# Kernel tuning notes

Measured on AMD Instinct MI355X. Metric: run time of the kernel, lower is better.

## Reference

```python
import jax, jax.numpy as jnp
import numpy as np

EPS = 1e-5  # equinox LayerNorm default eps

def setup_inputs() -> dict:
    key = jax.random.key(0)
    k1, k2, k3, k4, k5 = jax.random.split(key, 5)
    heads, d, dH, N = 16, 1024, 64, 2048
    # lecun-normal-ish scaling for fan_in=d
    s = 1.0 / np.sqrt(d)
    return {
        "x": jax.random.normal(k1, (d, N), dtype=jnp.float32),
        "WQ": jax.random.normal(k2, (heads, d, dH), dtype=jnp.float32) * s,
        "WK": jax.random.normal(k3, (heads, d, dH), dtype=jnp.float32) * s,
        "WV": jax.random.normal(k4, (heads, d, dH), dtype=jnp.float32) * s,
        "W0": jax.random.normal(k5, (d, d), dtype=jnp.float32) * s,
    }

def reference(x, WQ, WK, WV, W0):
    # x: [d, N]
    residual = x
    # equinox LayerNorm over full shape (d, N), no affine params
    mean = jnp.mean(x)
    var = jnp.var(x)
    xn = (x - mean) * jax.lax.rsqrt(var + EPS)
    # project: [h, d_model, dH] x [d_model, N] -> [h, dH, N]
    Q = jnp.einsum('hcd,ci->hdi', WQ, xn)
    K = jnp.einsum('hcd,ci->hdi', WK, xn)
    V = jnp.einsum('hcd,ci->hdi', WV, xn)
    dH = WK.shape[-1]
    dot = jnp.einsum('hdi,hdj->hij', Q, K)  # [h, N, N]
    alpha = jax.nn.softmax(dot / jnp.sqrt(jnp.asarray(dH, dot.dtype)), axis=-1)
    attn = jnp.einsum('hij,hdj->hdi', alpha, V)  # [h, dH, N]
    N = attn.shape[2]
    attn = attn.reshape(-1, N)  # [d, N]
    out = W0 @ attn
    return out + residual
```

## Files before the change

### kernel.cpp

```cpp
#include <hip/hip_runtime.h>
#include <math.h>

typedef unsigned short u16;
typedef _Float16 f16;
typedef __attribute__((ext_vector_type(8))) short bf16x8;
typedef __attribute__((ext_vector_type(4))) float f32x4;
typedef __attribute__((ext_vector_type(4))) f16 f16x4;

#define D_MODEL 1024
#define SEQ_N   2048
#define HEADS   16
#define DHEAD   64
#define M3      3072
#define NIT     (SEQ_N / 64)

#define GLOBAL_AS __attribute__((address_space(1)))
#define LDS_AS    __attribute__((address_space(3)))
#define ASYNC16(gp, lp) __builtin_amdgcn_global_load_lds( \
    (const GLOBAL_AS unsigned int*)(gp), (LDS_AS unsigned int*)(lp), 16, 0, 0)

__device__ __forceinline__ u16 f2bf(float f) {
  union { float f; unsigned int u; } v; v.f = f;
  unsigned int r = v.u + 0x7fffu + ((v.u >> 16) & 1u);
  return (u16)(r >> 16);
}

__global__ __launch_bounds__(256) void prep(const float* __restrict__ x,
                                            double* __restrict__ part,
                                            const float* __restrict__ WQ,
                                            const float* __restrict__ WK,
                                            const float* __restrict__ WV,
                                            const float* __restrict__ W0,
                                            u16* __restrict__ Wp,
                                            u16* __restrict__ W0p) {
  __shared__ double ls[256], lss[256];
  __shared__ float tile[32][65];
  int t = threadIdx.x;
  int b = blockIdx.x;
  if (b < 256) {
    const float4* x4 = (const float4*)x;
    const int n4 = (D_MODEL * SEQ_N) / 4;
    double s = 0.0, ss = 0.0;
    for (int idx = b * 256 + t; idx < n4; idx += 256 * 256) {
      float4 v = x4[idx];
      s  += (double)v.x + (double)v.y + (double)v.z + (double)v.w;
      ss += (double)v.x * v.x + (double)v.y * v.y + (double)v.z * v.z + (double)v.w * v.w;
    }
    ls[t] = s; lss[t] = ss;
    __syncthreads();
    for (int off = 128; off > 0; off >>= 1) {
      if (t < off) { ls[t] += ls[t + off]; lss[t] += lss[t + off]; }
      __syncthreads();
    }
    if (t == 0) { part[2 * b] = ls[0]; part[2 * b + 1] = lss[0]; }
    return;
  }
  int f = b - 256;
  int z = f >> 9;
  int rem = f & 511;
  if (z == 3) {
    int idx = rem * 512 + t;
#pragma unroll
    for (int r = 0; r < 2; ++r, idx += 256) {
      float4 v = ((const float4*)W0)[idx];
      unsigned int lo = (unsigned int)f2bf(v.x) | ((unsigned int)f2bf(v.y) << 16);
      unsigned int hi = (unsigned int)f2bf(v.z) | ((unsigned int)f2bf(v.w) << 16);
      uint2 o; o.x = lo; o.y = hi;
      *(uint2*)(&W0p[(size_t)idx * 4]) = o;
    }
    return;
  }
  const float* W = (z == 0) ? WQ : ((z == 1) ? WK : WV);
  int h = rem >> 5, cb = (rem & 31) * 32;
  int dh = t & 63, cl = t >> 6;
  for (int r = 0; r < 8; ++r) {
    int c = cl + r * 4;
    tile[c][dh] = W[((size_t)h * D_MODEL + cb + c) * DHEAD + dh];
  }
  __syncthreads();
  int c2 = t & 31, d2 = t >> 5;
  for (int r = 0; r < 8; ++r) {
    int dd = d2 + r * 8;
    Wp[(size_t)((z * HEADS + h) * DHEAD + dd) * D_MODEL + cb + c2] = f2bf(tile[c2][dd]);
  }
}

__global__ __launch_bounds__(256) void ln_norm_t(const float* __restrict__ x,
                                                 const double* __restrict__ part,
                                                 u16* __restrict__ xnt) {
  __shared__ double ls[256], lss[256];
  __shared__ float tile[64][65];
  int t = threadIdx.x;
  ls[t] = part[2 * t]; lss[t] = part[2 * t + 1];
  __syncthreads();
  for (int off = 128; off > 0; off >>= 1) {
    if (t < off) { ls[t] += ls[t + off]; lss[t] += lss[t + off]; }
    __syncthreads();
  }
  double inv = 1.0 / ((double)D_MODEL * (double)SEQ_N);
  double m = ls[0] * inv;
  double vv = lss[0] * inv - m * m;
  float mean = (float)m;
  float rstd = (float)(1.0 / sqrt(vv + 1e-5));

  int ib = blockIdx.x * 64, cb = blockIdx.y * 64;
  int il = t & 63, cl = t >> 6;
  for (int r = 0; r < 16; ++r) {
    int c = cl + r * 4;
    tile[c][il] = (x[(size_t)(cb + c) * SEQ_N + ib + il] - mean) * rstd;
  }
  __syncthreads();
  int c2 = t & 63, i2 = t >> 6;
  for (int r = 0; r < 16; ++r) {
    int i = i2 + r * 4;
    xnt[(size_t)(ib + i) * D_MODEL + cb + c2] = f2bf(tile[c2][i]);
  }
}

__global__ __launch_bounds__(256) void gemm_qkv(const u16* __restrict__ A,
                                                const u16* __restrict__ Bt,
                                                u16* __restrict__ Qt,
                                                u16* __restrict__ Kt,
                                                f16* __restrict__ Vb) {
  __shared__ __align__(16) u16 Alds[2 * 2 * 96 * 32];
  __shared__ __align__(16) u16 Blds[2 * 2 * 128 * 32];
  int t = threadIdx.x;
  int lane = t & 63, w = t >> 6;
  int g = lane >> 4, l16 = lane & 15;
  int wr = w >> 1, wc = w & 1;
  int flat = blockIdx.x;
  int wi = flat >> 3;
  int wx = wi & 7, wy = wi >> 3;
  int cx = (flat & 7) & 1, cy = (flat & 7) >> 1;
  int bx = cx * 8 + wx;
  int by = cy * 8 + wy;
  int mb = by * 96, nb = bx * 128;

  f32x4 acc[3][4];
#pragma unroll
  for (int i = 0; i < 3; ++i)
#pragma unroll
    for (int j = 0; j < 4; ++j) acc[i][j] = (f32x4){0.f, 0.f, 0.f, 0.f};

  const u16* AgP[3]; int ldsA[3];
#pragma unroll
  for (int r = 0; r < 3; ++r) {
    int idx = r * 256 + t;
    int kk = (idx >= 384) ? 1 : 0;
    int rem = idx - kk * 384;
    int row = rem >> 2, c4 = rem & 3;
    AgP[r] = A + (size_t)(mb + row) * D_MODEL + kk * 32 + c4 * 8;
    ldsA[r] = idx * 8;
  }
  const u16* BgP[4]; int ldsB[4];
#pragma unroll
  for (int r = 0; r < 4; ++r) {
    int idx = r * 256 + t;
    int kk = idx >> 9;
    int rem = idx & 511;
    int row = rem >> 2, c4 = rem & 3;
    BgP[r] = Bt + (size_t)(nb + row) * D_MODEL + kk * 32 + c4 * 8;
    ldsB[r] = idx * 8;
  }

#pragma unroll
  for (int r = 0; r < 3; ++r) ASYNC16(AgP[r], &Alds[ldsA[r]]);
#pragma unroll
  for (int r = 0; r < 4; ++r) ASYNC16(BgP[r], &Blds[ldsB[r]]);
#pragma unroll
  for (int r = 0; r < 3; ++r) ASYNC16(AgP[r] + 64, &Alds[6144 + ldsA[r]]);
#pragma unroll
  for (int r = 0; r < 4; ++r) ASYNC16(BgP[r] + 64, &Blds[8192 + ldsB[r]]);

  int cur = 0;
  for (int ks = 0; ks < 16; ++ks) {
    if (ks < 15) asm volatile("s_waitcnt vmcnt(7)" ::: "memory");
    else         asm volatile("s_waitcnt vmcnt(0)" ::: "memory");
    __builtin_amdgcn_s_barrier();
#pragma unroll
    for (int kk = 0; kk < 2; ++kk) {
      bf16x8 af[3], bf[4];
#pragma unroll
      for (int tm = 0; tm < 3; ++tm)
        af[tm] = *(const bf16x8*)(&Alds[cur * 6144 + kk * 3072 +
                                        (wr * 48 + tm * 16 + l16) * 32 + g * 8]);
#pragma unroll
      for (int tn = 0; tn < 4; ++tn)
        bf[tn] = *(const bf16x8*)(&Blds[cur * 8192 + kk * 4096 +
                                        (wc * 64 + tn * 16 + l16) * 32 + g * 8]);
#pragma unroll
      for (int tm = 0; tm < 3; ++tm)
#pragma unroll
        for (int tn = 0; tn < 4; ++tn)
          acc[tm][tn] = __builtin_amdgcn_mfma_f32_16x16x32_bf16(af[tm], bf[tn],
                                                                acc[tm][tn], 0, 0, 0);
    }
    __builtin_amdgcn_s_barrier();
    if (ks + 2 < 16) {
      int kb = (ks + 2) * 64;
#pragma unroll
      for (int r = 0; r < 3; ++r) ASYNC16(AgP[r] + kb, &Alds[cur * 6144 + ldsA[r]]);
#pragma unroll
      for (int r = 0; r < 4; ++r) ASYNC16(BgP[r] + kb, &Blds[cur * 8192 + ldsB[r]]);
    }
    cur ^= 1;
  }

#pragma unroll
  for (int tm = 0; tm < 3; ++tm) {
    int row0 = mb + wr * 48 + tm * 16 + g * 4;
#pragma unroll
    for (int tn = 0; tn < 4; ++tn) {
      int col = nb + wc * 64 + tn * 16 + l16;
      if (row0 < 2 * D_MODEL) {
        u16* T = (row0 < D_MODEL) ? Qt : Kt;
        int rbase = (row0 < D_MODEL) ? row0 : row0 - D_MODEL;
        ushort4 o;
        o.x = f2bf(acc[tm][tn][0]); o.y = f2bf(acc[tm][tn][1]);
        o.z = f2bf(acc[tm][tn][2]); o.w = f2bf(acc[tm][tn][3]);
        *(ushort4*)(&T[(size_t)col * D_MODEL + rbase]) = o;
      } else {
        int rbase = row0 - 2 * D_MODEL;
#pragma unroll
        for (int r = 0; r < 4; ++r)
          Vb[(size_t)(rbase + r) * SEQ_N + col] = (f16)acc[tm][tn][r];
      }
    }
  }
}

__global__ __launch_bounds__(256) void gemm_bf16(const u16* __restrict__ A,
                                                 const u16* __restrict__ Bt,
                                                 float* __restrict__ C,
                                                 const float* __restrict__ res,
                                                 int M, int N, int K) {
  __shared__ __align__(16) u16 Alds[2 * 2 * 64 * 32];
  __shared__ __align__(16) u16 Blds[2 * 2 * 64 * 32];
  int t = threadIdx.x;
  int w = t >> 6, lane = t & 63;
  int g = lane >> 4, l16 = lane & 15;
  int flat = blockIdx.x;
  int wi = flat >> 3;
  int wx = wi & 7, wy = wi >> 3;
  int cx = (flat & 7) & 3, cy = (flat & 7) >> 2;
  int bx = cx * 8 + wx;
  int by = cy * 8 + wy;
  int mb = by * 64, nb = bx * 64;
  f32x4 acc[4];
  for (int i = 0; i < 4; ++i) acc[i] = (f32x4){0.f, 0.f, 0.f, 0.f};

  const u16* AgP[2]; const u16* BgP[2]; int ldsO[2];
#pragma unroll
  for (int r = 0; r < 2; ++r) {
    int idx = r * 256 + t;
    int kk = idx >> 8;
    int rem = idx & 255;
    int row = rem >> 2, c4 = rem & 3;
    AgP[r] = A + (size_t)(mb + row) * K + kk * 32 + c4 * 8;
    BgP[r] = Bt + (size_t)(nb + row) * K + kk * 32 + c4 * 8;
    ldsO[r] = idx * 8;
  }

#pragma unroll
  for (int r = 0; r < 2; ++r) { ASYNC16(AgP[r], &Alds[ldsO[r]]); ASYNC16(BgP[r], &Blds[ldsO[r]]); }
#pragma unroll
  for (int r = 0; r < 2; ++r) {
    ASYNC16(AgP[r] + 64, &Alds[4096 + ldsO[r]]);
    ASYNC16(BgP[r] + 64, &Blds[4096 + ldsO[r]]);
  }

  int cur = 0;
  const int NK = 16;
  for (int ks = 0; ks < NK; ++ks) {
    if (ks < NK - 1) asm volatile("s_waitcnt vmcnt(4)" ::: "memory");
    else             asm volatile("s_waitcnt vmcnt(0)" ::: "memory");
    __builtin_amdgcn_s_barrier();
#pragma unroll
    for (int kk = 0; kk < 2; ++kk) {
      bf16x8 af = *(const bf16x8*)(&Alds[cur * 4096 + kk * 2048 + (w * 16 + l16) * 32 + g * 8]);
#pragma unroll
      for (int tn = 0; tn < 4; ++tn) {
        bf16x8 bf = *(const bf16x8*)(&Blds[cur * 4096 + kk * 2048 + (tn * 16 + l16) * 32 + g * 8]);
        acc[tn] = __builtin_amdgcn_mfma_f32_16x16x32_bf16(af, bf, acc[tn], 0, 0, 0);
      }
    }
    __builtin_amdgcn_s_barrier();
    if (ks + 2 < NK) {
      int kb = (ks + 2) * 64;
#pragma unroll
      for (int r = 0; r < 2; ++r) {
        ASYNC16(AgP[r] + kb, &Alds[cur * 4096 + ldsO[r]]);
        ASYNC16(BgP[r] + kb, &Blds[cur * 4096 + ldsO[r]]);
      }
    }
    cur ^= 1;
  }
  int col0 = nb + l16;
  int row0 = mb + w * 16 + g * 4;
#pragma unroll
  for (int tn = 0; tn < 4; ++tn) {
    int col = col0 + tn * 16;
#pragma unroll
    for (int r = 0; r < 4; ++r) {
      int row = row0 + r;
      float v = acc[tn][r];
      if (res) v += res[(size_t)row * N + col];
      C[(size_t)row * N + col] = v;
    }
  }
}

__global__ __launch_bounds__(256, 2) void attn_mfma(const u16* __restrict__ Qt,
                                                    const u16* __restrict__ Kt,
                                                    const f16* __restrict__ Vb,
                                                    u16* __restrict__ attnt) {
  __shared__ __align__(16) u16 Klds[2][64][72];
  __shared__ __align__(16) f16 Vlds[2][64][72];
  int flat = blockIdx.x;
  int xcd = flat & 7, idx = flat >> 3;
  int h  = xcd * 2 + (idx >> 5);
  int ib = (idx & 31) * 64;
  int t = threadIdx.x;
  int w = t >> 6, lane = t & 63;
  int g = lane >> 4, l16 = lane & 15;

  bf16x8 bq[2];
  {
    const u16* qb = Qt + (size_t)(ib + w * 16 + l16) * D_MODEL + h * DHEAD + g * 8;
    bq[0] = *(const bf16x8*)(qb);
    bq[1] = *(const bf16x8*)(qb + 32);
  }

  f32x4 acc_o[4];
#pragma unroll
  for (int i = 0; i < 4; ++i) acc_o[i] = (f32x4){0.f, 0.f, 0.f, 0.f};
  f32x4 acc_l = (f32x4){0.f, 0.f, 0.f, 0.f};
  f16x4 ones;
  ones[0] = (f16)1.f; ones[1] = (f16)1.f; ones[2] = (f16)1.f; ones[3] = (f16)1.f;

  int srow = t >> 2, sc0 = (t & 3) * 16;
  const u16* Kg = Kt + (size_t)srow * D_MODEL + h * DHEAD + sc0;
  const f16* Vg = Vb + (size_t)(h * DHEAD + srow) * SEQ_N + sc0;

  uint4 ka = *(const uint4*)(Kg);
  uint4 kb = *(const uint4*)(Kg + 8);
  uint4 va = *(const uint4*)(Vg);
  uint4 vb = *(const uint4*)(Vg + 8);
  *(uint4*)(&Klds[0][srow][sc0]) = ka;
  *(uint4*)(&Klds[0][srow][sc0 + 8]) = kb;
  *(uint4*)(&Vlds[0][srow][sc0]) = va;
  *(uint4*)(&Vlds[0][srow][sc0 + 8]) = vb;
  __syncthreads();

  int cur = 0;
  for (int it = 0; it < NIT; ++it) {
    if (it + 1 < NIT) {
      const u16* Kn = Kg + (size_t)(it + 1) * 64 * D_MODEL;
      const f16* Vn = Vg + (it + 1) * 64;
      ka = *(const uint4*)(Kn);
      kb = *(const uint4*)(Kn + 8);
      va = *(const uint4*)(Vn);
      vb = *(const uint4*)(Vn + 8);
    }

    f32x4 s[4];
#pragma unroll
    for (int i = 0; i < 4; ++i) s[i] = (f32x4){0.f, 0.f, 0.f, 0.f};
    __builtin_amdgcn_s_setprio(1);
#pragma unroll
    for (int kk = 0; kk < 2; ++kk)
#pragma unroll
      for (int tn = 0; tn < 4; ++tn) {
        bf16x8 ak = *(const bf16x8*)(&Klds[cur][tn * 16 + l16][kk * 32 + g * 8]);
        s[tn] = __builtin_amdgcn_mfma_f32_16x16x32_bf16(ak, bq[kk], s[tn], 0, 0, 0);
      }
    __builtin_amdgcn_s_setprio(0);
    f16x4 pf[4];
#pragma unroll
    for (int tn = 0; tn < 4; ++tn) {
      f16x4 p;
#pragma unroll
      for (int r = 0; r < 4; ++r)
        p[r] = (f16)__expf(fmaf(s[tn][r], 0.125f, -4.0f));
      pf[tn] = p;
    }
    __builtin_amdgcn_s_setprio(1);
#pragma unroll
    for (int tn = 0; tn < 4; ++tn) {
      acc_l = __builtin_amdgcn_mfma_f32_16x16x16f16(pf[tn], ones, acc_l, 0, 0, 0);
#pragma unroll
      for (int td = 0; td < 4; ++td) {
        f16x4 bv = *(const f16x4*)(&Vlds[cur][td * 16 + l16][tn * 16 + g * 4]);
        acc_o[td] =
            __builtin_amdgcn_mfma_f32_16x16x16f16(pf[tn], bv, acc_o[td], 0, 0, 0);
      }
    }
    __builtin_amdgcn_s_setprio(0);

    if (it + 1 < NIT) {
      *(uint4*)(&Klds[cur ^ 1][srow][sc0]) = ka;
      *(uint4*)(&Klds[cur ^ 1][srow][sc0 + 8]) = kb;
      *(uint4*)(&Vlds[cur ^ 1][srow][sc0]) = va;
      *(uint4*)(&Vlds[cur ^ 1][srow][sc0 + 8]) = vb;
    }
    __syncthreads();
    cur ^= 1;
  }

  float inv0 = 1.0f / acc_l[0];
  float inv1 = 1.0f / acc_l[1];
  float inv2 = 1.0f / acc_l[2];
  float inv3 = 1.0f / acc_l[3];
#pragma unroll
  for (int td = 0; td < 4; ++td) {
    int dh = h * DHEAD + td * 16 + l16;
    int i0 = ib + w * 16 + g * 4;
    attnt[(size_t)(i0 + 0) * D_MODEL + dh] = f2bf(acc_o[td][0] * inv0);
    attnt[(size_t)(i0 + 1) * D_MODEL + dh] = f2bf(acc_o[td][1] * inv1);
    attnt[(size_t)(i0 + 2) * D_MODEL + dh] = f2bf(acc_o[td][2] * inv2);
    attnt[(size_t)(i0 + 3) * D_MODEL + dh] = f2bf(acc_o[td][3] * inv3);
  }
}

extern "C" void kernel_launch(void* const* d_in, const int* in_sizes, int n_in,
                              void* d_out, int out_size, void* d_ws, size_t ws_size,
                              hipStream_t stream) {
  const float* x  = (const float*)d_in[0];
  const float* WQ = (const float*)d_in[1];
  const float* WK = (const float*)d_in[2];
  const float* WV = (const float*)d_in[3];
  const float* W0 = (const float*)d_in[4];
  float* out = (float*)d_out;

  char* ws = (char*)d_ws;
  size_t off = 0;
  double* part  = (double*)(ws + off); off += 8192;
  u16*    xnt   = (u16*)(ws + off); off += (size_t)SEQ_N * D_MODEL * 2;
  u16*    Wp    = (u16*)(ws + off); off += (size_t)M3 * D_MODEL * 2;
  u16*    W0p   = (u16*)(ws + off); off += (size_t)D_MODEL * D_MODEL * 2;
  u16*    Qt    = (u16*)(ws + off); off += (size_t)SEQ_N * D_MODEL * 2;
  u16*    Kt    = (u16*)(ws + off); off += (size_t)SEQ_N * D_MODEL * 2;
  f16*    Vb    = (f16*)(ws + off); off += (size_t)D_MODEL * SEQ_N * 2;
  u16*    attnt = (u16*)(ws + off); off += (size_t)SEQ_N * D_MODEL * 2;

  prep<<<256 + 2048, 256, 0, stream>>>(x, part, WQ, WK, WV, W0, Wp, W0p);
  ln_norm_t<<<dim3(SEQ_N / 64, D_MODEL / 64), 256, 0, stream>>>(x, part, xnt);
  gemm_qkv<<<512, 256, 0, stream>>>(Wp, xnt, Qt, Kt, Vb);
  attn_mfma<<<512, 256, 0, stream>>>(Qt, Kt, Vb, attnt);
  gemm_bf16<<<512, 256, 0, stream>>>(W0p, attnt, out, x, D_MODEL, SEQ_N, D_MODEL);
}
```

Before: 152.9 us.

## Fuse all five stages into one cooperative persistent kernel with grid syncs

Replaces the five separate kernel launches (stats/weight prep, layernorm transpose, QKV GEMM, attention, output GEMM) with a single cooperative kernel of 512 blocks that separates the stages with grid.sync(). The prep stage is reshaped so 512 blocks cover the stats and weight conversion work formerly spread over 2304 blocks. The aim is to remove per-launch overhead and the gaps between dependent kernels. In exchange, each stage is limited to 512 resident blocks with launch bounds allowing 2 per CU and a shared 56KB LDS buffer, and grid-wide barriers add their own cost. The old multi-kernel path is kept as a fallback if the cooperative launch fails.

```diff
diff --git a/kernel.cpp b/kernel.cpp
--- a/kernel.cpp
+++ b/kernel.cpp
@@ -1,5 +1,8 @@
 #include <hip/hip_runtime.h>
+#include <hip/hip_cooperative_groups.h>
 #include <math.h>
+
+namespace cg = cooperative_groups;
 
 typedef unsigned short u16;
 typedef _Float16 f16;
@@ -23,6 +26,406 @@
   union { float f; unsigned int u; } v; v.f = f;
   unsigned int r = v.u + 0x7fffu + ((v.u >> 16) & 1u);
   return (u16)(r >> 16);
+}
+
+__global__ __launch_bounds__(256, 2) void fused(
+    const float* __restrict__ x,  const float* __restrict__ WQ,
+    const float* __restrict__ WK, const float* __restrict__ WV,
+    const float* __restrict__ W0, float* __restrict__ out,
+    double* __restrict__ part, u16* __restrict__ xnt,
+    u16* __restrict__ Wp, u16* __restrict__ W0p,
+    u16* __restrict__ Qt, u16* __restrict__ Kt,
+    f16* __restrict__ Vb, u16* __restrict__ attnt) {
+  __shared__ __align__(16) char smem[57344];
+  cg::grid_group grid = cg::this_grid();
+  int b = blockIdx.x;
+  int t = threadIdx.x;
+
+  {
+    double* ls  = (double*)smem;
+    double* lss = ls + 256;
+    float*  tile = (float*)(smem + 4096);
+    if (b < 256) {
+      const float4* x4 = (const float4*)x;
+      const int n4 = (D_MODEL * SEQ_N) / 4;
+      double s = 0.0, ss = 0.0;
+      for (int idx = b * 256 + t; idx < n4; idx += 256 * 256) {
+        float4 v = x4[idx];
+        s  += (double)v.x + (double)v.y + (double)v.z + (double)v.w;
+        ss += (double)v.x * v.x + (double)v.y * v.y + (double)v.z * v.z + (double)v.w * v.w;
+      }
+      ls[t] = s; lss[t] = ss;
+      __syncthreads();
+      for (int off = 128; off > 0; off >>= 1) {
+        if (t < off) { ls[t] += ls[t + off]; lss[t] += lss[t + off]; }
+        __syncthreads();
+      }
+      if (t == 0) { part[2 * b] = ls[0]; part[2 * b + 1] = lss[0]; }
+    } else {
+      int base = (b - 256) * 8;
+      int z = base >> 9;
+      if (z == 3) {
+#pragma unroll
+        for (int u = 0; u < 8; ++u) {
+          int rem = (base + u) & 511;
+          int idx = rem * 512 + t;
+#pragma unroll
+          for (int r = 0; r < 2; ++r, idx += 256) {
+            float4 v = ((const float4*)W0)[idx];
+            unsigned int lo = (unsigned int)f2bf(v.x) | ((unsigned int)f2bf(v.y) << 16);
+            unsigned int hi = (unsigned int)f2bf(v.z) | ((unsigned int)f2bf(v.w) << 16);
+            uint2 o; o.x = lo; o.y = hi;
+            *(uint2*)(&W0p[(size_t)idx * 4]) = o;
+          }
+        }
+      } else {
+        const float* W = (z == 0) ? WQ : ((z == 1) ? WK : WV);
+        for (int u = 0; u < 8; ++u) {
+          int rem = (base + u) & 511;
+          int h = rem >> 5, cb = (rem & 31) * 32;
+          int dh = t & 63, cl = t >> 6;
+          for (int r = 0; r < 8; ++r) {
+            int c = cl + r * 4;
+            tile[c * 65 + dh] = W[((size_t)h * D_MODEL + cb + c) * DHEAD + dh];
+          }
+          __syncthreads();
+          int c2 = t & 31, d2 = t >> 5;
+          for (int r = 0; r < 8; ++r) {
+            int dd = d2 + r * 8;
+            Wp[(size_t)((z * HEADS + h) * DHEAD + dd) * D_MODEL + cb + c2] =
+                f2bf(tile[c2 * 65 + dd]);
+          }
+          __syncthreads();
+        }
+      }
+    }
+  }
+  grid.sync();
+
+  {
+    double* ls  = (double*)smem;
+    double* lss = ls + 256;
+    float*  tile = (float*)(smem + 4096);
+    ls[t] = part[2 * t]; lss[t] = part[2 * t + 1];
+    __syncthreads();
+    for (int off = 128; off > 0; off >>= 1) {
+      if (t < off) { ls[t] += ls[t + off]; lss[t] += lss[t + off]; }
+      __syncthreads();
+    }
+    double inv = 1.0 / ((double)D_MODEL * (double)SEQ_N);
+    double m = ls[0] * inv;
+    double vv = lss[0] * inv - m * m;
+    float mean = (float)m;
+    float rstd = (float)(1.0 / sqrt(vv + 1e-5));
+
+    int ib = (b & 31) * 64, cb = (b >> 5) * 64;
+    int il = t & 63, cl = t >> 6;
+    for (int r = 0; r < 16; ++r) {
+      int c = cl + r * 4;
+      tile[c * 65 + il] = (x[(size_t)(cb + c) * SEQ_N + ib + il] - mean) * rstd;
+    }
+    __syncthreads();
+    int c2 = t & 63, i2 = t >> 6;
+    for (int r = 0; r < 16; ++r) {
+      int i = i2 + r * 4;
+      xnt[(size_t)(ib + i) * D_MODEL + cb + c2] = f2bf(tile[c2 * 65 + i]);
+    }
+  }
+  grid.sync();
+
+  {
+    u16* Alds = (u16*)smem;
+    u16* Blds = (u16*)(smem + 24576);
+    int lane = t & 63, w = t >> 6;
+    int g = lane >> 4, l16 = lane & 15;
+    int wr = w >> 1, wc = w & 1;
+    int wi = b >> 3;
+    int wx = wi & 7, wy = wi >> 3;
+    int cx = (b & 7) & 1, cy = (b & 7) >> 1;
+    int bx = cx * 8 + wx;
+    int by = cy * 8 + wy;
+    int mb = by * 96, nb = bx * 128;
+
+    f32x4 acc[3][4];
+#pragma unroll
+    for (int i = 0; i < 3; ++i)
+#pragma unroll
+      for (int j = 0; j < 4; ++j) acc[i][j] = (f32x4){0.f, 0.f, 0.f, 0.f};
+
+    const u16* AgP[3]; int ldsA[3];
+#pragma unroll
+    for (int r = 0; r < 3; ++r) {
+      int idx = r * 256 + t;
+      int kk = (idx >= 384) ? 1 : 0;
+      int rem = idx - kk * 384;
+      int row = rem >> 2, c4 = rem & 3;
+      AgP[r] = Wp + (size_t)(mb + row) * D_MODEL + kk * 32 + c4 * 8;
+      ldsA[r] = idx * 8;
+    }
+    const u16* BgP[4]; int ldsB[4];
+#pragma unroll
+    for (int r = 0; r < 4; ++r) {
+      int idx = r * 256 + t;
+      int kk = idx >> 9;
+      int rem = idx & 511;
+      int row = rem >> 2, c4 = rem & 3;
+      BgP[r] = xnt + (size_t)(nb + row) * D_MODEL + kk * 32 + c4 * 8;
+      ldsB[r] = idx * 8;
+    }
+
+#pragma unroll
+    for (int r = 0; r < 3; ++r) ASYNC16(AgP[r], &Alds[ldsA[r]]);
+#pragma unroll
+    for (int r = 0; r < 4; ++r) ASYNC16(BgP[r], &Blds[ldsB[r]]);
+#pragma unroll
+    for (int r = 0; r < 3; ++r) ASYNC16(AgP[r] + 64, &Alds[6144 + ldsA[r]]);
+#pragma unroll
+    for (int r = 0; r < 4; ++r) ASYNC16(BgP[r] + 64, &Blds[8192 + ldsB[r]]);
+
+    int cur = 0;
+    for (int ks = 0; ks < 16; ++ks) {
+      if (ks < 15) asm volatile("s_waitcnt vmcnt(7)" ::: "memory");
+      else         asm volatile("s_waitcnt vmcnt(0)" ::: "memory");
+      __builtin_amdgcn_s_barrier();
+#pragma unroll
+      for (int kk = 0; kk < 2; ++kk) {
+        bf16x8 af[3], bf[4];
+#pragma unroll
+        for (int tm = 0; tm < 3; ++tm)
+          af[tm] = *(const bf16x8*)(&Alds[cur * 6144 + kk * 3072 +
+                                          (wr * 48 + tm * 16 + l16) * 32 + g * 8]);
+#pragma unroll
+        for (int tn = 0; tn < 4; ++tn)
+          bf[tn] = *(const bf16x8*)(&Blds[cur * 8192 + kk * 4096 +
+                                          (wc * 64 + tn * 16 + l16) * 32 + g * 8]);
+#pragma unroll
+        for (int tm = 0; tm < 3; ++tm)
+#pragma unroll
+          for (int tn = 0; tn < 4; ++tn)
+            acc[tm][tn] = __builtin_amdgcn_mfma_f32_16x16x32_bf16(af[tm], bf[tn],
+                                                                  acc[tm][tn], 0, 0, 0);
+      }
+      __builtin_amdgcn_s_barrier();
+      if (ks + 2 < 16) {
+        int kb = (ks + 2) * 64;
+#pragma unroll
+        for (int r = 0; r < 3; ++r) ASYNC16(AgP[r] + kb, &Alds[cur * 6144 + ldsA[r]]);
+#pragma unroll
+        for (int r = 0; r < 4; ++r) ASYNC16(BgP[r] + kb, &Blds[cur * 8192 + ldsB[r]]);
+      }
+      cur ^= 1;
+    }
+
+#pragma unroll
+    for (int tm = 0; tm < 3; ++tm) {
+      int row0 = mb + wr * 48 + tm * 16 + g * 4;
+#pragma unroll
+      for (int tn = 0; tn < 4; ++tn) {
+        int col = nb + wc * 64 + tn * 16 + l16;
+        if (row0 < 2 * D_MODEL) {
+          u16* T = (row0 < D_MODEL) ? Qt : Kt;
+          int rbase = (row0 < D_MODEL) ? row0 : row0 - D_MODEL;
+          ushort4 o;
+          o.x = f2bf(acc[tm][tn][0]); o.y = f2bf(acc[tm][tn][1]);
+          o.z = f2bf(acc[tm][tn][2]); o.w = f2bf(acc[tm][tn][3]);
+          *(ushort4*)(&T[(size_t)col * D_MODEL + rbase]) = o;
+        } else {
+          int rbase = row0 - 2 * D_MODEL;
+#pragma unroll
+          for (int r = 0; r < 4; ++r)
+            Vb[(size_t)(rbase + r) * SEQ_N + col] = (f16)acc[tm][tn][r];
+        }
+      }
+    }
+  }
+  grid.sync();
+
+  {
+    u16* Klds = (u16*)smem;
+    f16* Vlds = (f16*)(smem + 18432);
+#define KLD(bf_, r_, c_) Klds[(bf_)*4608 + (r_)*72 + (c_)]
+#define VLD(bf_, r_, c_) Vlds[(bf_)*4608 + (r_)*72 + (c_)]
+    int xcd = b & 7, idx = b >> 3;
+    int h  = xcd * 2 + (idx >> 5);
+    int ib = (idx & 31) * 64;
+    int w = t >> 6, lane = t & 63;
+    int g = lane >> 4, l16 = lane & 15;
+
+    bf16x8 bq[2];
+    {
+      const u16* qb = Qt + (size_t)(ib + w * 16 + l16) * D_MODEL + h * DHEAD + g * 8;
+      bq[0] = *(const bf16x8*)(qb);
+      bq[1] = *(const bf16x8*)(qb + 32);
+    }
+
+    f32x4 acc_o[4];
+#pragma unroll
+    for (int i = 0; i < 4; ++i) acc_o[i] = (f32x4){0.f, 0.f, 0.f, 0.f};
+    f32x4 acc_l = (f32x4){0.f, 0.f, 0.f, 0.f};
+    f16x4 ones;
+    ones[0] = (f16)1.f; ones[1] = (f16)1.f; ones[2] = (f16)1.f; ones[3] = (f16)1.f;
+
+    int srow = t >> 2, sc0 = (t & 3) * 16;
+    const u16* Kg = Kt + (size_t)srow * D_MODEL + h * DHEAD + sc0;
+    const f16* Vg = Vb + (size_t)(h * DHEAD + srow) * SEQ_N + sc0;
+
+    uint4 ka = *(const uint4*)(Kg);
+    uint4 kb = *(const uint4*)(Kg + 8);
+    uint4 va = *(const uint4*)(Vg);
+    uint4 vb = *(const uint4*)(Vg + 8);
+    *(uint4*)(&KLD(0, srow, sc0)) = ka;
+    *(uint4*)(&KLD(0, srow, sc0 + 8)) = kb;
+    *(uint4*)(&VLD(0, srow, sc0)) = va;
+    *(uint4*)(&VLD(0, srow, sc0 + 8)) = vb;
+    __syncthreads();
+
+    int cur = 0;
+    for (int it = 0; it < NIT; ++it) {
+      if (it + 1 < NIT) {
+        const u16* Kn = Kg + (size_t)(it + 1) * 64 * D_MODEL;
+        const f16* Vn = Vg + (it + 1) * 64;
+        ka = *(const uint4*)(Kn);
+        kb = *(const uint4*)(Kn + 8);
+        va = *(const uint4*)(Vn);
+        vb = *(const uint4*)(Vn + 8);
+      }
+
+      f32x4 s[4];
+#pragma unroll
+      for (int i = 0; i < 4; ++i) s[i] = (f32x4){0.f, 0.f, 0.f, 0.f};
+      __builtin_amdgcn_s_setprio(1);
+#pragma unroll
+      for (int kk = 0; kk < 2; ++kk)
+#pragma unroll
+        for (int tn = 0; tn < 4; ++tn) {
+          bf16x8 ak = *(const bf16x8*)(&KLD(cur, tn * 16 + l16, kk * 32 + g * 8));
+          s[tn] = __builtin_amdgcn_mfma_f32_16x16x32_bf16(ak, bq[kk], s[tn], 0, 0, 0);
+        }
+      __builtin_amdgcn_s_setprio(0);
+      f16x4 pf[4];
+#pragma unroll
+      for (int tn = 0; tn < 4; ++tn) {
+        f16x4 p;
+#pragma unroll
+        for (int r = 0; r < 4; ++r)
+          p[r] = (f16)__expf(fmaf(s[tn][r], 0.125f, -4.0f));
+        pf[tn] = p;
+      }
+      __builtin_amdgcn_s_setprio(1);
+#pragma unroll
+      for (int tn = 0; tn < 4; ++tn) {
+        acc_l = __builtin_amdgcn_mfma_f32_16x16x16f16(pf[tn], ones, acc_l, 0, 0, 0);
+#pragma unroll
+        for (int td = 0; td < 4; ++td) {
+          f16x4 bv = *(const f16x4*)(&VLD(cur, td * 16 + l16, tn * 16 + g * 4));
+          acc_o[td] =
+              __builtin_amdgcn_mfma_f32_16x16x16f16(pf[tn], bv, acc_o[td], 0, 0, 0);
+        }
+      }
+      __builtin_amdgcn_s_setprio(0);
+
+      if (it + 1 < NIT) {
+        *(uint4*)(&KLD(cur ^ 1, srow, sc0)) = ka;
+        *(uint4*)(&KLD(cur ^ 1, srow, sc0 + 8)) = kb;
+        *(uint4*)(&VLD(cur ^ 1, srow, sc0)) = va;
+        *(uint4*)(&VLD(cur ^ 1, srow, sc0 + 8)) = vb;
+      }
+      __syncthreads();
+      cur ^= 1;
+    }
+
+    float inv0 = 1.0f / acc_l[0];
+    float inv1 = 1.0f / acc_l[1];
+    float inv2 = 1.0f / acc_l[2];
+    float inv3 = 1.0f / acc_l[3];
+#pragma unroll
+    for (int td = 0; td < 4; ++td) {
+      int dh = h * DHEAD + td * 16 + l16;
+      int i0 = ib + w * 16 + g * 4;
+      attnt[(size_t)(i0 + 0) * D_MODEL + dh] = f2bf(acc_o[td][0] * inv0);
+      attnt[(size_t)(i0 + 1) * D_MODEL + dh] = f2bf(acc_o[td][1] * inv1);
+      attnt[(size_t)(i0 + 2) * D_MODEL + dh] = f2bf(acc_o[td][2] * inv2);
+      attnt[(size_t)(i0 + 3) * D_MODEL + dh] = f2bf(acc_o[td][3] * inv3);
+    }
+#undef KLD
+#undef VLD
+  }
+  grid.sync();
+
+  {
+    u16* Alds = (u16*)smem;
+    u16* Blds = (u16*)(smem + 16384);
+    int w = t >> 6, lane = t & 63;
+    int g = lane >> 4, l16 = lane & 15;
+    int wi = b >> 3;
+    int wx = wi & 7, wy = wi >> 3;
+    int cx = (b & 7) & 3, cy = (b & 7) >> 2;
+    int bx = cx * 8 + wx;
+    int by = cy * 8 + wy;
+    int mb = by * 64, nb = bx * 64;
+    f32x4 acc[4];
+    for (int i = 0; i < 4; ++i) acc[i] = (f32x4){0.f, 0.f, 0.f, 0.f};
+
+    const u16* AgP[2]; const u16* BgP[2]; int ldsO[2];
+#pragma unroll
+    for (int r = 0; r < 2; ++r) {
+      int idx = r * 256 + t;
+      int kk = idx >> 8;
+      int rem = idx & 255;
+      int row = rem >> 2, c4 = rem & 3;
+      AgP[r] = W0p + (size_t)(mb + row) * D_MODEL + kk * 32 + c4 * 8;
+      BgP[r] = attnt + (size_t)(nb + row) * D_MODEL + kk * 32 + c4 * 8;
+      ldsO[r] = idx * 8;
+    }
+
+#pragma unroll
+    for (int r = 0; r < 2; ++r) { ASYNC16(AgP[r], &Alds[ldsO[r]]); ASYNC16(BgP[r], &Blds[ldsO[r]]); }
+#pragma unroll
+    for (int r = 0; r < 2; ++r) {
+      ASYNC16(AgP[r] + 64, &Alds[4096 + ldsO[r]]);
+      ASYNC16(BgP[r] + 64, &Blds[4096 + ldsO[r]]);
+    }
+
+    int cur = 0;
+    const int NK = 16;
+    for (int ks = 0; ks < NK; ++ks) {
+      if (ks < NK - 1) asm volatile("s_waitcnt vmcnt(4)" ::: "memory");
+      else             asm volatile("s_waitcnt vmcnt(0)" ::: "memory");
+      __builtin_amdgcn_s_barrier();
+#pragma unroll
+      for (int kk = 0; kk < 2; ++kk) {
+        bf16x8 af = *(const bf16x8*)(&Alds[cur * 4096 + kk * 2048 + (w * 16 + l16) * 32 + g * 8]);
+#pragma unroll
+        for (int tn = 0; tn < 4; ++tn) {
+          bf16x8 bf = *(const bf16x8*)(&Blds[cur * 4096 + kk * 2048 + (tn * 16 + l16) * 32 + g * 8]);
+          acc[tn] = __builtin_amdgcn_mfma_f32_16x16x32_bf16(af, bf, acc[tn], 0, 0, 0);
+        }
+      }
+      __builtin_amdgcn_s_barrier();
+      if (ks + 2 < NK) {
+        int kb = (ks + 2) * 64;
+#pragma unroll
+        for (int r = 0; r < 2; ++r) {
+          ASYNC16(AgP[r] + kb, &Alds[cur * 4096 + ldsO[r]]);
+          ASYNC16(BgP[r] + kb, &Blds[cur * 4096 + ldsO[r]]);
+        }
+      }
+      cur ^= 1;
+    }
+    int col0 = nb + l16;
+    int row0 = mb + w * 16 + g * 4;
+#pragma unroll
+    for (int tn = 0; tn < 4; ++tn) {
+      int col = col0 + tn * 16;
+#pragma unroll
+      for (int r = 0; r < 4; ++r) {
+        int row = row0 + r;
+        float v = acc[tn][r];
+        v += x[(size_t)row * SEQ_N + col];
+        out[(size_t)row * SEQ_N + col] = v;
+      }
+    }
+  }
 }
 
 __global__ __launch_bounds__(256) void prep(const float* __restrict__ x,
@@ -443,9 +846,15 @@
   f16*    Vb    = (f16*)(ws + off); off += (size_t)D_MODEL * SEQ_N * 2;
   u16*    attnt = (u16*)(ws + off); off += (size_t)SEQ_N * D_MODEL * 2;
 
-  prep<<<256 + 2048, 256, 0, stream>>>(x, part, WQ, WK, WV, W0, Wp, W0p);
-  ln_norm_t<<<dim3(SEQ_N / 64, D_MODEL / 64), 256, 0, stream>>>(x, part, xnt);
-  gemm_qkv<<<512, 256, 0, stream>>>(Wp, xnt, Qt, Kt, Vb);
-  attn_mfma<<<512, 256, 0, stream>>>(Qt, Kt, Vb, attnt);
-  gemm_bf16<<<512, 256, 0, stream>>>(W0p, attnt, out, x, D_MODEL, SEQ_N, D_MODEL);
+  void* args[] = {&x, &WQ, &WK, &WV, &W0, &out,
+                  &part, &xnt, &Wp, &W0p, &Qt, &Kt, &Vb, &attnt};
+  hipError_t err = hipLaunchCooperativeKernel((const void*)fused, dim3(512), dim3(256),
+                                              args, 0, stream);
+  if (err != hipSuccess) {
+    prep<<<256 + 2048, 256, 0, stream>>>(x, part, WQ, WK, WV, W0, Wp, W0p);
+    ln_norm_t<<<dim3(SEQ_N / 64, D_MODEL / 64), 256, 0, stream>>>(x, part, xnt);
+    gemm_qkv<<<512, 256, 0, stream>>>(Wp, xnt, Qt, Kt, Vb);
+    attn_mfma<<<512, 256, 0, stream>>>(Qt, Kt, Vb, attnt);
+    gemm_bf16<<<512, 256, 0, stream>>>(W0p, attnt, out, x, D_MODEL, SEQ_N, D_MODEL);
+  }
 }
```

After: 400.1 us. 2.62x slower.
